# Kernel tuning notes

Measured on AMD Instinct MI355X. Metric: run time of the kernel, lower is better.

The kernel has to match this reference:

```python
import jax, jax.numpy as jnp
import numpy as np

B, N, D, KD = 8, 2048, 64, 64

def setup_inputs() -> dict:
    key = jax.random.key(0)
    ks = jax.random.split(key, 7)
    s = 1.0 / np.sqrt(D)
    return {
        "x":  jax.random.normal(ks[0], (B, N, D), dtype=jnp.float32),
        "Wq": jax.random.normal(ks[1], (D, KD), dtype=jnp.float32) * s,
        "bq": jnp.zeros((KD,), jnp.float32),
        "Wk": jax.random.normal(ks[2], (D, KD), dtype=jnp.float32) * s,
        "bk": jnp.zeros((KD,), jnp.float32),
        "Wv": jax.random.normal(ks[3], (D, KD), dtype=jnp.float32) * s,
        "bv": jnp.zeros((KD,), jnp.float32),
    }

def reference(x, Wq, bq, Wk, bk, Wv, bv):
    # Q,K,V: [B,N,KD]
    Q = x @ Wq + bq
    K = x @ Wk + bk
    V = x @ Wv + bv
    # scores: [B,N,N] (note: original applies NO 1/sqrt(d) scaling)
    scores = jnp.einsum('bij,bkj->bik', Q, K)
    probs = jax.nn.softmax(scores, axis=-1)
    # mean-threshold sparsification: keep entries above the row mean
    mask = (probs > jnp.mean(probs, axis=-1, keepdims=True)).astype(probs.dtype)
    sparse = probs * mask
    out = jnp.einsum('bij,bjk->bik', sparse, V)  # [B,N,KD]
    return out
```

## Files before the change

### kernel.cpp

```cpp
#include <hip/hip_runtime.h>

#define NB 8
#define NS 2048
#define ND 64
#define LOG2E 1.44269504f

typedef _Float16 half8 __attribute__((ext_vector_type(8)));
typedef _Float16 half4 __attribute__((ext_vector_type(4)));
typedef __attribute__((ext_vector_type(4))) float floatx4;

__device__ __forceinline__ half8 cvt8(const float* p) {
    float4 a = *(const float4*)p;
    float4 b = *(const float4*)(p + 4);
    half8 h = {(_Float16)a.x, (_Float16)a.y, (_Float16)a.z, (_Float16)a.w,
               (_Float16)b.x, (_Float16)b.y, (_Float16)b.z, (_Float16)b.w};
    return h;
}

__global__ __launch_bounds__(256) void wprep(
    const float* __restrict__ Wq, const float* __restrict__ Wk,
    const float* __restrict__ Wv, _Float16* __restrict__ Wt)
{
    const int m = blockIdx.x;
    const float* W = (m == 0) ? Wq : (m == 1) ? Wk : Wv;
    for (int i = threadIdx.x; i < 64 * 64; i += 256) {
        const int c = i >> 6, d = i & 63;
        Wt[((size_t)m * 64 + c) * 64 + d] = (_Float16)W[d * 64 + c];
    }
}

__global__ __launch_bounds__(256) void qkv_proj(
    const float* __restrict__ x, const _Float16* __restrict__ Wt,
    const float* __restrict__ bq, const float* __restrict__ bk,
    const float* __restrict__ bv,
    _Float16* __restrict__ Qg, _Float16* __restrict__ Kg,
    _Float16* __restrict__ Vt)
{
    __shared__ _Float16 vt[4][64 * 20];

    const int tid  = threadIdx.x;
    const int wv   = tid >> 6;
    const int l    = tid & 63;
    const int quad = l >> 4;
    const int tx   = l & 15;

    const int b  = blockIdx.x & 7;
    const int n0 = (blockIdx.x >> 3) * 64 + wv * 16;

    const float* xr = x + ((size_t)b * NS + n0 + tx) * ND + quad * 8;
    half8 a0 = cvt8(xr);
    half8 a1 = cvt8(xr + 32);

    const floatx4 zf = {0.f, 0.f, 0.f, 0.f};

#pragma unroll
    for (int ctile = 0; ctile < 12; ++ctile) {
        const int m    = ctile >> 2;
        const int lcol = (ctile & 3) * 16 + tx;

        const _Float16* Wb = Wt + ((size_t)m * 64 + lcol) * 64;
        half8 b0 = *(const half8*)(Wb + quad * 8);
        half8 b1 = *(const half8*)(Wb + 32 + quad * 8);

        floatx4 acc = __builtin_amdgcn_mfma_f32_16x16x32_f16(a0, b0, zf, 0, 0, 0);
        acc = __builtin_amdgcn_mfma_f32_16x16x32_f16(a1, b1, acc, 0, 0, 0);

        const float* Bp = (m == 0) ? bq : (m == 1) ? bk : bv;
        const float bias = Bp[lcol];

        if (m == 0) {
#pragma unroll
            for (int r = 0; r < 4; ++r)
                Qg[((size_t)b * NS + n0 + quad * 4 + r) * ND + lcol] =
                    (_Float16)((acc[r] + bias) * LOG2E);
        } else if (m == 1) {
#pragma unroll
            for (int r = 0; r < 4; ++r)
                Kg[((size_t)b * NS + n0 + quad * 4 + r) * ND + lcol] =
                    (_Float16)(acc[r] + bias);
        } else {
#pragma unroll
            for (int r = 0; r < 4; ++r)
                vt[wv][lcol * 20 + quad * 4 + r] = (_Float16)(acc[r] + bias);
        }
    }
    __syncthreads();
    {
        const int d = l;
        const _Float16* src = &vt[wv][d * 20];
        uint2 p0 = *(const uint2*)(src);
        uint2 p1 = *(const uint2*)(src + 4);
        uint2 p2 = *(const uint2*)(src + 8);
        uint2 p3 = *(const uint2*)(src + 12);
        uint4 q0 = {p0.x, p0.y, p1.x, p1.y};
        uint4 q1 = {p2.x, p2.y, p3.x, p3.y};
        _Float16* dst = Vt + ((size_t)b * ND + d) * NS + n0;
        *(uint4*)(dst)     = q0;
        *(uint4*)(dst + 8) = q1;
    }
}

__global__ __launch_bounds__(512, 2) void attn(
    const _Float16* __restrict__ Qg,
    const _Float16* __restrict__ Kg,
    const _Float16* __restrict__ Vt,
    float* __restrict__ out)
{
    __shared__ __align__(16) _Float16 smem[2 * 64 * 72 + 2 * 64 * 72];
    __shared__ float lsh[4 * 64];

    _Float16* ksm = smem;
    _Float16* vsm = smem + 2 * 64 * 72;

    const int tid  = threadIdx.x;
    const int wv   = tid >> 6;
    const int l    = tid & 63;
    const int quad = l >> 4;
    const int tx   = l & 15;
    const int h    = wv >> 2;
    const int kq   = wv & 3;

    const int b  = blockIdx.x & 7;
    const int q0 = (blockIdx.x >> 3) * 64;

    const _Float16* Qb = Qg + ((size_t)b * NS + q0 + h * 32) * ND;
    const _Float16* Kb = Kg + (size_t)b * NS * ND;
    const _Float16* Vb = Vt + (size_t)b * ND * NS;

    half8 qf[2][2];
#pragma unroll
    for (int rh = 0; rh < 2; ++rh)
#pragma unroll
        for (int kc = 0; kc < 2; ++kc)
            qf[rh][kc] = *(const half8*)(Qb + (size_t)(rh * 16 + tx) * ND + kc * 32 + quad * 8);

    const int skey = tid >> 3;
    const int sc   = (tid & 7) * 8;
    const _Float16* Ksrc = Kb + (size_t)skey * ND + sc;
    const _Float16* Vsrc = Vb + (size_t)skey * NS + sc;
    const int kdst = skey * 72 + sc;

    const floatx4 zf = {0.f, 0.f, 0.f, 0.f};
    const int krow = (kq * 16 + tx) * 72;

    float lacc0 = 0.f, lacc1 = 0.f;
    {
        uint4 gk = *(const uint4*)Ksrc;
        *(uint4*)(ksm + kdst) = gk;
        for (int t = 0; t < 32; ++t) {
            const int buf = (t & 1) * 4608;
            __syncthreads();
            if (t < 31) gk = *(const uint4*)(Ksrc + (size_t)(t + 1) * 64 * ND);
            half8 kf0 = *(const half8*)(ksm + buf + krow + quad * 8);
            half8 kf1 = *(const half8*)(ksm + buf + krow + 32 + quad * 8);
#pragma unroll
            for (int rh = 0; rh < 2; ++rh) {
                floatx4 c = __builtin_amdgcn_mfma_f32_16x16x32_f16(kf0, qf[rh][0], zf, 0, 0, 0);
                c = __builtin_amdgcn_mfma_f32_16x16x32_f16(kf1, qf[rh][1], c, 0, 0, 0);
                float ladd = __builtin_amdgcn_exp2f(c[0]) + __builtin_amdgcn_exp2f(c[1])
                           + __builtin_amdgcn_exp2f(c[2]) + __builtin_amdgcn_exp2f(c[3]);
                if (rh == 0) lacc0 += ladd; else lacc1 += ladd;
            }
            if (t < 31) *(uint4*)(ksm + (buf ^ 4608) + kdst) = gk;
        }
    }
#pragma unroll
    for (int off = 16; off < 64; off <<= 1) {
        lacc0 += __shfl_xor(lacc0, off);
        lacc1 += __shfl_xor(lacc1, off);
    }
    if (quad == 0) {
        lsh[kq * 64 + h * 32 + tx]      = lacc0;
        lsh[kq * 64 + h * 32 + 16 + tx] = lacc1;
    }

    uint4 gk = *(const uint4*)Ksrc;
    uint4 gv = *(const uint4*)Vsrc;
    __syncthreads();

    float thr0, inv0, thr1, inv1;
    {
        const int row = h * 32 + tx;
        float L0 = lsh[row] + lsh[64 + row] + lsh[128 + row] + lsh[192 + row];
        float L1 = lsh[row + 16] + lsh[64 + row + 16] + lsh[128 + row + 16] + lsh[192 + row + 16];
        inv0 = 1.f / L0;  thr0 = L0 * (1.f / (float)NS);
        inv1 = 1.f / L1;  thr1 = L1 * (1.f / (float)NS);
    }

    *(uint4*)(ksm + kdst) = gk;
    *(uint4*)(vsm + kdst) = gv;

    floatx4 o[2][4] = {{zf, zf, zf, zf}, {zf, zf, zf, zf}};

    for (int t = 0; t < 32; ++t) {
        const int buf = (t & 1) * 4608;
        __syncthreads();
        if (t < 31) {
            gk = *(const uint4*)(Ksrc + (size_t)(t + 1) * 64 * ND);
            gv = *(const uint4*)(Vsrc + (size_t)(t + 1) * 64);
        }
        half8 kf0 = *(const half8*)(ksm + buf + krow + quad * 8);
        half8 kf1 = *(const half8*)(ksm + buf + krow + 32 + quad * 8);
        half4 vf[4];
#pragma unroll
        for (int dg = 0; dg < 4; ++dg)
            vf[dg] = *(const half4*)(vsm + buf + (dg * 16 + tx) * 72 + kq * 16 + quad * 4);
#pragma unroll
        for (int rh = 0; rh < 2; ++rh) {
            floatx4 c = __builtin_amdgcn_mfma_f32_16x16x32_f16(kf0, qf[rh][0], zf, 0, 0, 0);
            c = __builtin_amdgcn_mfma_f32_16x16x32_f16(kf1, qf[rh][1], c, 0, 0, 0);
            const float thr = rh ? thr1 : thr0;
            const float inv = rh ? inv1 : inv0;
            float e0 = __builtin_amdgcn_exp2f(c[0]);
            float e1 = __builtin_amdgcn_exp2f(c[1]);
            float e2 = __builtin_amdgcn_exp2f(c[2]);
            float e3 = __builtin_amdgcn_exp2f(c[3]);
            float w0 = (e0 > thr) ? e0 * inv : 0.f;
            float w1 = (e1 > thr) ? e1 * inv : 0.f;
            float w2 = (e2 > thr) ? e2 * inv : 0.f;
            float w3 = (e3 > thr) ? e3 * inv : 0.f;
            half4 af = {(_Float16)w0, (_Float16)w1, (_Float16)w2, (_Float16)w3};
#pragma unroll
            for (int dg = 0; dg < 4; ++dg)
                o[rh][dg] = __builtin_amdgcn_mfma_f32_16x16x16f16(af, vf[dg], o[rh][dg], 0, 0, 0);
        }
        if (t < 31) {
            *(uint4*)(ksm + (buf ^ 4608) + kdst) = gk;
            *(uint4*)(vsm + (buf ^ 4608) + kdst) = gv;
        }
    }

    __syncthreads();
    float* osm = (float*)smem;
    if (kq == 0) {
#pragma unroll
        for (int rh = 0; rh < 2; ++rh)
#pragma unroll
            for (int dg = 0; dg < 4; ++dg)
#pragma unroll
                for (int r = 0; r < 4; ++r)
                    osm[(h * 32 + rh * 16 + quad * 4 + r) * 68 + dg * 16 + tx] = o[rh][dg][r];
    }
    __syncthreads();
    if (kq == 1) {
#pragma unroll
        for (int rh = 0; rh < 2; ++rh)
#pragma unroll
            for (int dg = 0; dg < 4; ++dg)
#pragma unroll
                for (int r = 0; r < 4; ++r)
                    osm[(h * 32 + rh * 16 + quad * 4 + r) * 68 + dg * 16 + tx] += o[rh][dg][r];
    }
    __syncthreads();
    if (kq == 2) {
#pragma unroll
        for (int rh = 0; rh < 2; ++rh)
#pragma unroll
            for (int dg = 0; dg < 4; ++dg)
#pragma unroll
                for (int r = 0; r < 4; ++r)
                    osm[(h * 32 + rh * 16 + quad * 4 + r) * 68 + dg * 16 + tx] += o[rh][dg][r];
    }
    __syncthreads();
    if (kq == 3) {
#pragma unroll
        for (int rh = 0; rh < 2; ++rh)
#pragma unroll
            for (int dg = 0; dg < 4; ++dg)
#pragma unroll
                for (int r = 0; r < 4; ++r)
                    out[((size_t)b * NS + q0 + h * 32 + rh * 16 + quad * 4 + r) * ND + dg * 16 + tx] =
                        osm[(h * 32 + rh * 16 + quad * 4 + r) * 68 + dg * 16 + tx] + o[rh][dg][r];
    }
}

extern "C" void kernel_launch(void* const* d_in, const int* in_sizes, int n_in,
                              void* d_out, int out_size, void* d_ws, size_t ws_size,
                              hipStream_t stream) {
    const float* x  = (const float*)d_in[0];
    const float* Wq = (const float*)d_in[1];
    const float* bq = (const float*)d_in[2];
    const float* Wk = (const float*)d_in[3];
    const float* bk = (const float*)d_in[4];
    const float* Wv = (const float*)d_in[5];
    const float* bv = (const float*)d_in[6];

    _Float16* Qg = (_Float16*)d_ws;
    _Float16* Kg = Qg + (size_t)NB * NS * ND;
    _Float16* Vt = Kg + (size_t)NB * NS * ND;
    _Float16* Wt = Vt + (size_t)NB * NS * ND;

    wprep<<<3, 256, 0, stream>>>(Wq, Wk, Wv, Wt);
    qkv_proj<<<NB * (NS / 64), 256, 0, stream>>>(x, Wt, bq, bk, bv, Qg, Kg, Vt);
    attn<<<NB * (NS / 64), 512, 0, stream>>>(Qg, Kg, Vt, (float*)d_out);
}
```

Measured before the change: 112.4 us.

## Cache quantized scores in LDS to skip recomputing QK^T in second pass

The first pass now stores each wave's attention scores as 16-bit fixed-point integers (scale 256) in a per-wave LDS buffer. The second pass reads them back instead of recomputing Q·K^T. K and V are loaded straight from global memory into registers with double-buffered prefetch rather than staged through shared LDS tiles, and each block handles 32 query rows with 8 waves splitting the keys. This removes the second QK MFMA pass and the per-tile barriers, at the cost of about 135KB of LDS per block (likely one block per CU), quantization error in the scores, a clamp at ±125 in the log2 domain, and a tree reduction across 8 waves.

```diff
diff --git a/kernel.cpp b/kernel.cpp
--- a/kernel.cpp
+++ b/kernel.cpp
@@ -4,6 +4,8 @@
 #define NS 2048
 #define ND 64
 #define LOG2E 1.44269504f
+#define QSC 256.0f
+#define IQS (1.0f / 256.0f)
 
 typedef _Float16 half8 __attribute__((ext_vector_type(8)));
 typedef _Float16 half4 __attribute__((ext_vector_type(4)));
@@ -106,26 +108,24 @@
     const _Float16* __restrict__ Vt,
     float* __restrict__ out)
 {
-    __shared__ __align__(16) _Float16 smem[2 * 64 * 72 + 2 * 64 * 72];
-    __shared__ float lsh[4 * 64];
-
-    _Float16* ksm = smem;
-    _Float16* vsm = smem + 2 * 64 * 72;
+    __shared__ short psl[8][32 * 264];
+    __shared__ float lsh[32 * 8];
 
     const int tid  = threadIdx.x;
     const int wv   = tid >> 6;
     const int l    = tid & 63;
     const int quad = l >> 4;
     const int tx   = l & 15;
-    const int h    = wv >> 2;
+    const int e    = wv >> 2;
     const int kq   = wv & 3;
 
     const int b  = blockIdx.x & 7;
-    const int q0 = (blockIdx.x >> 3) * 64;
-
-    const _Float16* Qb = Qg + ((size_t)b * NS + q0 + h * 32) * ND;
+    const int q0 = (blockIdx.x >> 3) * 32;
+
+    const _Float16* Qb = Qg + ((size_t)b * NS + q0) * ND;
     const _Float16* Kb = Kg + (size_t)b * NS * ND;
     const _Float16* Vb = Vt + (size_t)b * ND * NS;
+    short* ps = psl[wv];
 
     half8 qf[2][2];
 #pragma unroll
@@ -134,34 +134,44 @@
         for (int kc = 0; kc < 2; ++kc)
             qf[rh][kc] = *(const half8*)(Qb + (size_t)(rh * 16 + tx) * ND + kc * 32 + quad * 8);
 
-    const int skey = tid >> 3;
-    const int sc   = (tid & 7) * 8;
-    const _Float16* Ksrc = Kb + (size_t)skey * ND + sc;
-    const _Float16* Vsrc = Vb + (size_t)skey * NS + sc;
-    const int kdst = skey * 72 + sc;
-
     const floatx4 zf = {0.f, 0.f, 0.f, 0.f};
-    const int krow = (kq * 16 + tx) * 72;
+
+    const _Float16* Kw = Kb + ((size_t)(e * 64 + kq * 16 + tx)) * ND;
 
     float lacc0 = 0.f, lacc1 = 0.f;
     {
-        uint4 gk = *(const uint4*)Ksrc;
-        *(uint4*)(ksm + kdst) = gk;
-        for (int t = 0; t < 32; ++t) {
-            const int buf = (t & 1) * 4608;
-            __syncthreads();
-            if (t < 31) gk = *(const uint4*)(Ksrc + (size_t)(t + 1) * 64 * ND);
-            half8 kf0 = *(const half8*)(ksm + buf + krow + quad * 8);
-            half8 kf1 = *(const half8*)(ksm + buf + krow + 32 + quad * 8);
+        half8 kf0[2], kf1[2];
+        kf0[0] = *(const half8*)(Kw + quad * 8);
+        kf1[0] = *(const half8*)(Kw + 32 + quad * 8);
+        kf0[1] = *(const half8*)(Kw + (size_t)128 * ND + quad * 8);
+        kf1[1] = *(const half8*)(Kw + (size_t)128 * ND + 32 + quad * 8);
+#pragma unroll
+        for (int tl = 0; tl < 16; ++tl) {
+            const int sl = tl & 1;
+            half8 a0 = kf0[sl], a1 = kf1[sl];
+            if (tl < 14) {
+                kf0[sl] = *(const half8*)(Kw + (size_t)(tl + 2) * 128 * ND + quad * 8);
+                kf1[sl] = *(const half8*)(Kw + (size_t)(tl + 2) * 128 * ND + 32 + quad * 8);
+            }
 #pragma unroll
             for (int rh = 0; rh < 2; ++rh) {
-                floatx4 c = __builtin_amdgcn_mfma_f32_16x16x32_f16(kf0, qf[rh][0], zf, 0, 0, 0);
-                c = __builtin_amdgcn_mfma_f32_16x16x32_f16(kf1, qf[rh][1], c, 0, 0, 0);
-                float ladd = __builtin_amdgcn_exp2f(c[0]) + __builtin_amdgcn_exp2f(c[1])
-                           + __builtin_amdgcn_exp2f(c[2]) + __builtin_amdgcn_exp2f(c[3]);
+                floatx4 c = __builtin_amdgcn_mfma_f32_16x16x32_f16(a0, qf[rh][0], zf, 0, 0, 0);
+                c = __builtin_amdgcn_mfma_f32_16x16x32_f16(a1, qf[rh][1], c, 0, 0, 0);
+                int ic[4];
+                float ladd = 0.f;
+#pragma unroll
+                for (int r = 0; r < 4; ++r) {
+                    float cs = fminf(fmaxf(c[r] * QSC, -32000.f), 32000.f);
+                    int v = (int)rintf(cs);
+                    ic[r] = v;
+                    ladd += __builtin_amdgcn_exp2f((float)v * IQS);
+                }
                 if (rh == 0) lacc0 += ladd; else lacc1 += ladd;
-            }
-            if (t < 31) *(uint4*)(ksm + (buf ^ 4608) + kdst) = gk;
+                uint2 pk;
+                pk.x = (unsigned)(ic[0] & 0xffff) | ((unsigned)ic[1] << 16);
+                pk.y = (unsigned)(ic[2] & 0xffff) | ((unsigned)ic[3] << 16);
+                *(uint2*)&ps[(rh * 16 + tx) * 264 + tl * 16 + quad * 4] = pk;
+            }
         }
     }
 #pragma unroll
@@ -170,107 +180,152 @@
         lacc1 += __shfl_xor(lacc1, off);
     }
     if (quad == 0) {
-        lsh[kq * 64 + h * 32 + tx]      = lacc0;
-        lsh[kq * 64 + h * 32 + 16 + tx] = lacc1;
-    }
-
-    uint4 gk = *(const uint4*)Ksrc;
-    uint4 gv = *(const uint4*)Vsrc;
+        lsh[tx * 8 + wv]        = lacc0;
+        lsh[(16 + tx) * 8 + wv] = lacc1;
+    }
     __syncthreads();
 
     float thr0, inv0, thr1, inv1;
     {
-        const int row = h * 32 + tx;
-        float L0 = lsh[row] + lsh[64 + row] + lsh[128 + row] + lsh[192 + row];
-        float L1 = lsh[row + 16] + lsh[64 + row + 16] + lsh[128 + row + 16] + lsh[192 + row + 16];
+        float4 s0a = *(const float4*)&lsh[tx * 8];
+        float4 s0b = *(const float4*)&lsh[tx * 8 + 4];
+        float4 s1a = *(const float4*)&lsh[(16 + tx) * 8];
+        float4 s1b = *(const float4*)&lsh[(16 + tx) * 8 + 4];
+        float L0 = s0a.x + s0a.y + s0a.z + s0a.w + s0b.x + s0b.y + s0b.z + s0b.w;
+        float L1 = s1a.x + s1a.y + s1a.z + s1a.w + s1b.x + s1b.y + s1b.z + s1b.w;
         inv0 = 1.f / L0;  thr0 = L0 * (1.f / (float)NS);
         inv1 = 1.f / L1;  thr1 = L1 * (1.f / (float)NS);
     }
 
-    *(uint4*)(ksm + kdst) = gk;
-    *(uint4*)(vsm + kdst) = gv;
+    const _Float16* Vw = Vb + (size_t)tx * NS + e * 64 + kq * 16 + quad * 4;
 
     floatx4 o[2][4] = {{zf, zf, zf, zf}, {zf, zf, zf, zf}};
-
-    for (int t = 0; t < 32; ++t) {
-        const int buf = (t & 1) * 4608;
-        __syncthreads();
-        if (t < 31) {
-            gk = *(const uint4*)(Ksrc + (size_t)(t + 1) * 64 * ND);
-            gv = *(const uint4*)(Vsrc + (size_t)(t + 1) * 64);
+    {
+        uint2 P0[2], P1[2];
+        half4 Vf[2][4];
+        P0[0] = *(const uint2*)&ps[tx * 264 + quad * 4];
+        P1[0] = *(const uint2*)&ps[(16 + tx) * 264 + quad * 4];
+        P0[1] = *(const uint2*)&ps[tx * 264 + 16 + quad * 4];
+        P1[1] = *(const uint2*)&ps[(16 + tx) * 264 + 16 + quad * 4];
+#pragma unroll
+        for (int dg = 0; dg < 4; ++dg) {
+            Vf[0][dg] = *(const half4*)(Vw + (size_t)(dg * 16) * NS);
+            Vf[1][dg] = *(const half4*)(Vw + (size_t)(dg * 16) * NS + 128);
         }
-        half8 kf0 = *(const half8*)(ksm + buf + krow + quad * 8);
-        half8 kf1 = *(const half8*)(ksm + buf + krow + 32 + quad * 8);
-        half4 vf[4];
-#pragma unroll
-        for (int dg = 0; dg < 4; ++dg)
-            vf[dg] = *(const half4*)(vsm + buf + (dg * 16 + tx) * 72 + kq * 16 + quad * 4);
-#pragma unroll
-        for (int rh = 0; rh < 2; ++rh) {
-            floatx4 c = __builtin_amdgcn_mfma_f32_16x16x32_f16(kf0, qf[rh][0], zf, 0, 0, 0);
-            c = __builtin_amdgcn_mfma_f32_16x16x32_f16(kf1, qf[rh][1], c, 0, 0, 0);
-            const float thr = rh ? thr1 : thr0;
-            const float inv = rh ? inv1 : inv0;
-            float e0 = __builtin_amdgcn_exp2f(c[0]);
-            float e1 = __builtin_amdgcn_exp2f(c[1]);
-            float e2 = __builtin_amdgcn_exp2f(c[2]);
-            float e3 = __builtin_amdgcn_exp2f(c[3]);
-            float w0 = (e0 > thr) ? e0 * inv : 0.f;
-            float w1 = (e1 > thr) ? e1 * inv : 0.f;
-            float w2 = (e2 > thr) ? e2 * inv : 0.f;
-            float w3 = (e3 > thr) ? e3 * inv : 0.f;
-            half4 af = {(_Float16)w0, (_Float16)w1, (_Float16)w2, (_Float16)w3};
-#pragma unroll
-            for (int dg = 0; dg < 4; ++dg)
-                o[rh][dg] = __builtin_amdgcn_mfma_f32_16x16x16f16(af, vf[dg], o[rh][dg], 0, 0, 0);
+#pragma unroll
+        for (int tl = 0; tl < 16; ++tl) {
+            const int sl = tl & 1;
+            uint2 u0 = P0[sl], u1 = P1[sl];
+            half4 v0 = Vf[sl][0], v1 = Vf[sl][1], v2 = Vf[sl][2], v3 = Vf[sl][3];
+            if (tl < 14) {
+                P0[sl] = *(const uint2*)&ps[tx * 264 + (tl + 2) * 16 + quad * 4];
+                P1[sl] = *(const uint2*)&ps[(16 + tx) * 264 + (tl + 2) * 16 + quad * 4];
+#pragma unroll
+                for (int dg = 0; dg < 4; ++dg)
+                    Vf[sl][dg] = *(const half4*)(Vw + (size_t)(dg * 16) * NS + (tl + 2) * 128);
+            }
+            half4 af0, af1;
+            {
+                int s0 = (int)(short)(u0.x), s1 = (int)(short)(u0.x >> 16);
+                int s2 = (int)(short)(u0.y), s3 = (int)(short)(u0.y >> 16);
+                float e0 = __builtin_amdgcn_exp2f((float)s0 * IQS);
+                float e1 = __builtin_amdgcn_exp2f((float)s1 * IQS);
+                float e2 = __builtin_amdgcn_exp2f((float)s2 * IQS);
+                float e3 = __builtin_amdgcn_exp2f((float)s3 * IQS);
+                af0[0] = (_Float16)((e0 > thr0) ? e0 * inv0 : 0.f);
+                af0[1] = (_Float16)((e1 > thr0) ? e1 * inv0 : 0.f);
+                af0[2] = (_Float16)((e2 > thr0) ? e2 * inv0 : 0.f);
+                af0[3] = (_Float16)((e3 > thr0) ? e3 * inv0 : 0.f);
+            }
+            {
+                int s0 = (int)(short)(u1.x), s1 = (int)(short)(u1.x >> 16);
+                int s2 = (int)(short)(u1.y), s3 = (int)(short)(u1.y >> 16);
+                float e0 = __builtin_amdgcn_exp2f((float)s0 * IQS);
+                float e1 = __builtin_amdgcn_exp2f((float)s1 * IQS);
+                float e2 = __builtin_amdgcn_exp2f((float)s2 * IQS);
+                float e3 = __builtin_amdgcn_exp2f((float)s3 * IQS);
+                af1[0] = (_Float16)((e0 > thr1) ? e0 * inv1 : 0.f);
+                af1[1] = (_Float16)((e1 > thr1) ? e1 * inv1 : 0.f);
+                af1[2] = (_Float16)((e2 > thr1) ? e2 * inv1 : 0.f);
+                af1[3] = (_Float16)((e3 > thr1) ? e3 * inv1 : 0.f);
+            }
+            o[0][0] = __builtin_amdgcn_mfma_f32_16x16x16f16(af0, v0, o[0][0], 0, 0, 0);
+            o[0][1] = __builtin_amdgcn_mfma_f32_16x16x16f16(af0, v1, o[0][1], 0, 0, 0);
+            o[0][2] = __builtin_amdgcn_mfma_f32_16x16x16f16(af0, v2, o[0][2], 0, 0, 0);
+            o[0][3] = __builtin_amdgcn_mfma_f32_16x16x16f16(af0, v3, o[0][3], 0, 0, 0);
+            o[1][0] = __builtin_amdgcn_mfma_f32_16x16x16f16(af1, v0, o[1][0], 0, 0, 0);
+            o[1][1] = __builtin_amdgcn_mfma_f32_16x16x16f16(af1, v1, o[1][1], 0, 0, 0);
+            o[1][2] = __builtin_amdgcn_mfma_f32_16x16x16f16(af1, v2, o[1][2], 0, 0, 0);
+            o[1][3] = __builtin_amdgcn_mfma_f32_16x16x16f16(af1, v3, o[1][3], 0, 0, 0);
         }
-        if (t < 31) {
-            *(uint4*)(ksm + (buf ^ 4608) + kdst) = gk;
-            *(uint4*)(vsm + (buf ^ 4608) + kdst) = gv;
-        }
-    }
-
-    __syncthreads();
-    float* osm = (float*)smem;
-    if (kq == 0) {
-#pragma unroll
-        for (int rh = 0; rh < 2; ++rh)
-#pragma unroll
-            for (int dg = 0; dg < 4; ++dg)
-#pragma unroll
-                for (int r = 0; r < 4; ++r)
-                    osm[(h * 32 + rh * 16 + quad * 4 + r) * 68 + dg * 16 + tx] = o[rh][dg][r];
-    }
-    __syncthreads();
-    if (kq == 1) {
-#pragma unroll
-        for (int rh = 0; rh < 2; ++rh)
-#pragma unroll
-            for (int dg = 0; dg < 4; ++dg)
-#pragma unroll
-                for (int r = 0; r < 4; ++r)
-                    osm[(h * 32 + rh * 16 + quad * 4 + r) * 68 + dg * 16 + tx] += o[rh][dg][r];
-    }
-    __syncthreads();
-    if (kq == 2) {
-#pragma unroll
-        for (int rh = 0; rh < 2; ++rh)
-#pragma unroll
-            for (int dg = 0; dg < 4; ++dg)
-#pragma unroll
-                for (int r = 0; r < 4; ++r)
-                    osm[(h * 32 + rh * 16 + quad * 4 + r) * 68 + dg * 16 + tx] += o[rh][dg][r];
-    }
-    __syncthreads();
-    if (kq == 3) {
-#pragma unroll
-        for (int rh = 0; rh < 2; ++rh)
-#pragma unroll
-            for (int dg = 0; dg < 4; ++dg)
-#pragma unroll
-                for (int r = 0; r < 4; ++r)
-                    out[((size_t)b * NS + q0 + h * 32 + rh * 16 + quad * 4 + r) * ND + dg * 16 + tx] =
-                        osm[(h * 32 + rh * 16 + quad * 4 + r) * 68 + dg * 16 + tx] + o[rh][dg][r];
+    }
+
+    __syncthreads();
+    float* osm = (float*)&psl[0][0];
+    if (wv >= 4) {
+        float* s = osm + (size_t)(wv - 4) * 32 * 68;
+#pragma unroll
+        for (int rh = 0; rh < 2; ++rh)
+#pragma unroll
+            for (int dg = 0; dg < 4; ++dg)
+#pragma unroll
+                for (int r = 0; r < 4; ++r)
+                    s[(rh * 16 + quad * 4 + r) * 68 + dg * 16 + tx] = o[rh][dg][r];
+    }
+    __syncthreads();
+    if (wv < 4) {
+        const float* s = osm + (size_t)wv * 32 * 68;
+#pragma unroll
+        for (int rh = 0; rh < 2; ++rh)
+#pragma unroll
+            for (int dg = 0; dg < 4; ++dg)
+#pragma unroll
+                for (int r = 0; r < 4; ++r)
+                    o[rh][dg][r] += s[(rh * 16 + quad * 4 + r) * 68 + dg * 16 + tx];
+    }
+    __syncthreads();
+    if (wv == 2 || wv == 3) {
+        float* s = osm + (size_t)(wv - 2) * 32 * 68;
+#pragma unroll
+        for (int rh = 0; rh < 2; ++rh)
+#pragma unroll
+            for (int dg = 0; dg < 4; ++dg)
+#pragma unroll
+                for (int r = 0; r < 4; ++r)
+                    s[(rh * 16 + quad * 4 + r) * 68 + dg * 16 + tx] = o[rh][dg][r];
+    }
+    __syncthreads();
+    if (wv < 2) {
+        const float* s = osm + (size_t)wv * 32 * 68;
+#pragma unroll
+        for (int rh = 0; rh < 2; ++rh)
+#pragma unroll
+            for (int dg = 0; dg < 4; ++dg)
+#pragma unroll
+                for (int r = 0; r < 4; ++r)
+                    o[rh][dg][r] += s[(rh * 16 + quad * 4 + r) * 68 + dg * 16 + tx];
+    }
+    __syncthreads();
+    if (wv == 1) {
+        float* s = osm;
+#pragma unroll
+        for (int rh = 0; rh < 2; ++rh)
+#pragma unroll
+            for (int dg = 0; dg < 4; ++dg)
+#pragma unroll
+                for (int r = 0; r < 4; ++r)
+                    s[(rh * 16 + quad * 4 + r) * 68 + dg * 16 + tx] = o[rh][dg][r];
+    }
+    __syncthreads();
+    if (wv == 0) {
+#pragma unroll
+        for (int rh = 0; rh < 2; ++rh)
+#pragma unroll
+            for (int dg = 0; dg < 4; ++dg)
+#pragma unroll
+                for (int r = 0; r < 4; ++r)
+                    out[((size_t)b * NS + q0 + rh * 16 + quad * 4 + r) * ND + dg * 16 + tx] =
+                        o[rh][dg][r] + osm[(rh * 16 + quad * 4 + r) * 68 + dg * 16 + tx];
     }
 }
 
@@ -292,5 +347,5 @@
 
     wprep<<<3, 256, 0, stream>>>(Wq, Wk, Wv, Wt);
     qkv_proj<<<NB * (NS / 64), 256, 0, stream>>>(x, Wt, bq, bk, bv, Qg, Kg, Vt);
-    attn<<<NB * (NS / 64), 512, 0, stream>>>(Qg, Kg, Vt, (float*)d_out);
-}
+    attn<<<NB * (NS / 32), 512, 0, stream>>>(Qg, Kg, Vt, (float*)d_out);
+}
```

Result: slower. 127.4 us (+13.4%).

## Halve query tile per block and XOR-swizzle K/V shared memory

Applied to the files above, without the earlier changes.

The attention kernel now handles 32 query rows per block instead of 64, which doubles the grid to 512 blocks and has each wave own a single 16-row slice. That should spread work across more CUs, but each K/V tile is now loaded from global memory by twice as many blocks. K and V tiles are stored in shared memory with an XOR swizzle on 8-element chunks, with matching swizzled read offsets, to reduce LDS bank conflicts. Per-thread registers drop because the accumulators and Q fragments shrink by half.

```diff
diff --git a/kernel.cpp b/kernel.cpp
--- a/kernel.cpp
+++ b/kernel.cpp
@@ -107,7 +107,7 @@
     float* __restrict__ out)
 {
     __shared__ __align__(16) _Float16 smem[2 * 64 * 72 + 2 * 64 * 72];
-    __shared__ float lsh[4 * 64];
+    __shared__ float lsh[4 * 32];
 
     _Float16* ksm = smem;
     _Float16* vsm = smem + 2 * 64 * 72;
@@ -117,80 +117,74 @@
     const int l    = tid & 63;
     const int quad = l >> 4;
     const int tx   = l & 15;
-    const int h    = wv >> 2;
+    const int rh   = wv >> 2;
     const int kq   = wv & 3;
 
     const int b  = blockIdx.x & 7;
-    const int q0 = (blockIdx.x >> 3) * 64;
-
-    const _Float16* Qb = Qg + ((size_t)b * NS + q0 + h * 32) * ND;
+    const int q0 = (blockIdx.x >> 3) * 32;
+
+    const _Float16* Qb = Qg + ((size_t)b * NS + q0 + rh * 16) * ND;
     const _Float16* Kb = Kg + (size_t)b * NS * ND;
     const _Float16* Vb = Vt + (size_t)b * ND * NS;
 
-    half8 qf[2][2];
-#pragma unroll
-    for (int rh = 0; rh < 2; ++rh)
-#pragma unroll
-        for (int kc = 0; kc < 2; ++kc)
-            qf[rh][kc] = *(const half8*)(Qb + (size_t)(rh * 16 + tx) * ND + kc * 32 + quad * 8);
+    half8 qf[2];
+#pragma unroll
+    for (int kc = 0; kc < 2; ++kc)
+        qf[kc] = *(const half8*)(Qb + (size_t)tx * ND + kc * 32 + quad * 8);
 
     const int skey = tid >> 3;
-    const int sc   = (tid & 7) * 8;
-    const _Float16* Ksrc = Kb + (size_t)skey * ND + sc;
-    const _Float16* Vsrc = Vb + (size_t)skey * NS + sc;
-    const int kdst = skey * 72 + sc;
+    const int sc   = tid & 7;
+    const _Float16* Ksrc = Kb + (size_t)skey * ND + sc * 8;
+    const _Float16* Vsrc = Vb + (size_t)skey * NS + sc * 8;
+    const int sdst = skey * 72 + ((sc ^ (skey & 7)) * 8);
 
     const floatx4 zf = {0.f, 0.f, 0.f, 0.f};
-    const int krow = (kq * 16 + tx) * 72;
-
-    float lacc0 = 0.f, lacc1 = 0.f;
+    const int t7    = tx & 7;
+    const int krow  = (kq * 16 + tx) * 72;
+    const int koff0 = (quad ^ t7) * 8;
+    const int koff1 = ((quad ^ 4) ^ t7) * 8;
+
+    float lacc = 0.f;
     {
         uint4 gk = *(const uint4*)Ksrc;
-        *(uint4*)(ksm + kdst) = gk;
+        *(uint4*)(ksm + sdst) = gk;
         for (int t = 0; t < 32; ++t) {
             const int buf = (t & 1) * 4608;
             __syncthreads();
             if (t < 31) gk = *(const uint4*)(Ksrc + (size_t)(t + 1) * 64 * ND);
-            half8 kf0 = *(const half8*)(ksm + buf + krow + quad * 8);
-            half8 kf1 = *(const half8*)(ksm + buf + krow + 32 + quad * 8);
-#pragma unroll
-            for (int rh = 0; rh < 2; ++rh) {
-                floatx4 c = __builtin_amdgcn_mfma_f32_16x16x32_f16(kf0, qf[rh][0], zf, 0, 0, 0);
-                c = __builtin_amdgcn_mfma_f32_16x16x32_f16(kf1, qf[rh][1], c, 0, 0, 0);
-                float ladd = __builtin_amdgcn_exp2f(c[0]) + __builtin_amdgcn_exp2f(c[1])
-                           + __builtin_amdgcn_exp2f(c[2]) + __builtin_amdgcn_exp2f(c[3]);
-                if (rh == 0) lacc0 += ladd; else lacc1 += ladd;
-            }
-            if (t < 31) *(uint4*)(ksm + (buf ^ 4608) + kdst) = gk;
-        }
-    }
-#pragma unroll
-    for (int off = 16; off < 64; off <<= 1) {
-        lacc0 += __shfl_xor(lacc0, off);
-        lacc1 += __shfl_xor(lacc1, off);
-    }
-    if (quad == 0) {
-        lsh[kq * 64 + h * 32 + tx]      = lacc0;
-        lsh[kq * 64 + h * 32 + 16 + tx] = lacc1;
-    }
+            half8 kf0 = *(const half8*)(ksm + buf + krow + koff0);
+            half8 kf1 = *(const half8*)(ksm + buf + krow + koff1);
+            floatx4 c = __builtin_amdgcn_mfma_f32_16x16x32_f16(kf0, qf[0], zf, 0, 0, 0);
+            c = __builtin_amdgcn_mfma_f32_16x16x32_f16(kf1, qf[1], c, 0, 0, 0);
+            lacc += __builtin_amdgcn_exp2f(c[0]) + __builtin_amdgcn_exp2f(c[1])
+                  + __builtin_amdgcn_exp2f(c[2]) + __builtin_amdgcn_exp2f(c[3]);
+            if (t < 31) *(uint4*)(ksm + (buf ^ 4608) + sdst) = gk;
+        }
+    }
+#pragma unroll
+    for (int off = 16; off < 64; off <<= 1)
+        lacc += __shfl_xor(lacc, off);
+    if (quad == 0)
+        lsh[kq * 32 + rh * 16 + tx] = lacc;
 
     uint4 gk = *(const uint4*)Ksrc;
     uint4 gv = *(const uint4*)Vsrc;
     __syncthreads();
 
-    float thr0, inv0, thr1, inv1;
+    float thr, inv;
     {
-        const int row = h * 32 + tx;
-        float L0 = lsh[row] + lsh[64 + row] + lsh[128 + row] + lsh[192 + row];
-        float L1 = lsh[row + 16] + lsh[64 + row + 16] + lsh[128 + row + 16] + lsh[192 + row + 16];
-        inv0 = 1.f / L0;  thr0 = L0 * (1.f / (float)NS);
-        inv1 = 1.f / L1;  thr1 = L1 * (1.f / (float)NS);
-    }
-
-    *(uint4*)(ksm + kdst) = gk;
-    *(uint4*)(vsm + kdst) = gv;
-
-    floatx4 o[2][4] = {{zf, zf, zf, zf}, {zf, zf, zf, zf}};
+        const int row = rh * 16 + tx;
+        float L = lsh[row] + lsh[32 + row] + lsh[64 + row] + lsh[96 + row];
+        inv = 1.f / L;
+        thr = L * (1.f / (float)NS);
+    }
+
+    *(uint4*)(ksm + sdst) = gk;
+    *(uint4*)(vsm + sdst) = gv;
+
+    const int vchunk = ((kq * 2 + (quad >> 1)) ^ t7) * 8 + (quad & 1) * 4;
+
+    floatx4 o[4] = {zf, zf, zf, zf};
 
     for (int t = 0; t < 32; ++t) {
         const int buf = (t & 1) * 4608;
@@ -199,78 +193,68 @@
             gk = *(const uint4*)(Ksrc + (size_t)(t + 1) * 64 * ND);
             gv = *(const uint4*)(Vsrc + (size_t)(t + 1) * 64);
         }
-        half8 kf0 = *(const half8*)(ksm + buf + krow + quad * 8);
-        half8 kf1 = *(const half8*)(ksm + buf + krow + 32 + quad * 8);
+        half8 kf0 = *(const half8*)(ksm + buf + krow + koff0);
+        half8 kf1 = *(const half8*)(ksm + buf + krow + koff1);
         half4 vf[4];
 #pragma unroll
         for (int dg = 0; dg < 4; ++dg)
-            vf[dg] = *(const half4*)(vsm + buf + (dg * 16 + tx) * 72 + kq * 16 + quad * 4);
-#pragma unroll
-        for (int rh = 0; rh < 2; ++rh) {
-            floatx4 c = __builtin_amdgcn_mfma_f32_16x16x32_f16(kf0, qf[rh][0], zf, 0, 0, 0);
-            c = __builtin_amdgcn_mfma_f32_16x16x32_f16(kf1, qf[rh][1], c, 0, 0, 0);
-            const float thr = rh ? thr1 : thr0;
-            const float inv = rh ? inv1 : inv0;
-            float e0 = __builtin_amdgcn_exp2f(c[0]);
-            float e1 = __builtin_amdgcn_exp2f(c[1]);
-            float e2 = __builtin_amdgcn_exp2f(c[2]);
-            float e3 = __builtin_amdgcn_exp2f(c[3]);
-            float w0 = (e0 > thr) ? e0 * inv : 0.f;
-            float w1 = (e1 > thr) ? e1 * inv : 0.f;
-            float w2 = (e2 > thr) ? e2 * inv : 0.f;
-            float w3 = (e3 > thr) ? e3 * inv : 0.f;
-            half4 af = {(_Float16)w0, (_Float16)w1, (_Float16)w2, (_Float16)w3};
-#pragma unroll
-            for (int dg = 0; dg < 4; ++dg)
-                o[rh][dg] = __builtin_amdgcn_mfma_f32_16x16x16f16(af, vf[dg], o[rh][dg], 0, 0, 0);
-        }
+            vf[dg] = *(const half4*)(vsm + buf + (dg * 16 + tx) * 72 + vchunk);
+
+        floatx4 c = __builtin_amdgcn_mfma_f32_16x16x32_f16(kf0, qf[0], zf, 0, 0, 0);
+        c = __builtin_amdgcn_mfma_f32_16x16x32_f16(kf1, qf[1], c, 0, 0, 0);
+        float e0 = __builtin_amdgcn_exp2f(c[0]);
+        float e1 = __builtin_amdgcn_exp2f(c[1]);
+        float e2 = __builtin_amdgcn_exp2f(c[2]);
+        float e3 = __builtin_amdgcn_exp2f(c[3]);
+        float w0 = (e0 > thr) ? e0 * inv : 0.f;
+        float w1 = (e1 > thr) ? e1 * inv : 0.f;
+        float w2 = (e2 > thr) ? e2 * inv : 0.f;
+        float w3 = (e3 > thr) ? e3 * inv : 0.f;
+        half4 af = {(_Float16)w0, (_Float16)w1, (_Float16)w2, (_Float16)w3};
+#pragma unroll
+        for (int dg = 0; dg < 4; ++dg)
+            o[dg] = __builtin_amdgcn_mfma_f32_16x16x16f16(af, vf[dg], o[dg], 0, 0, 0);
+
         if (t < 31) {
-            *(uint4*)(ksm + (buf ^ 4608) + kdst) = gk;
-            *(uint4*)(vsm + (buf ^ 4608) + kdst) = gv;
+            *(uint4*)(ksm + (buf ^ 4608) + sdst) = gk;
+            *(uint4*)(vsm + (buf ^ 4608) + sdst) = gv;
         }
     }
 
     __syncthreads();
     float* osm = (float*)smem;
+    const int orow = rh * 16 + quad * 4;
     if (kq == 0) {
 #pragma unroll
-        for (int rh = 0; rh < 2; ++rh)
-#pragma unroll
-            for (int dg = 0; dg < 4; ++dg)
-#pragma unroll
-                for (int r = 0; r < 4; ++r)
-                    osm[(h * 32 + rh * 16 + quad * 4 + r) * 68 + dg * 16 + tx] = o[rh][dg][r];
+        for (int dg = 0; dg < 4; ++dg)
+#pragma unroll
+            for (int r = 0; r < 4; ++r)
+                osm[(orow + r) * 68 + dg * 16 + tx] = o[dg][r];
     }
     __syncthreads();
     if (kq == 1) {
 #pragma unroll
-        for (int rh = 0; rh < 2; ++rh)
-#pragma unroll
-            for (int dg = 0; dg < 4; ++dg)
-#pragma unroll
-                for (int r = 0; r < 4; ++r)
-                    osm[(h * 32 + rh * 16 + quad * 4 + r) * 68 + dg * 16 + tx] += o[rh][dg][r];
+        for (int dg = 0; dg < 4; ++dg)
+#pragma unroll
+            for (int r = 0; r < 4; ++r)
+                osm[(orow + r) * 68 + dg * 16 + tx] += o[dg][r];
     }
     __syncthreads();
     if (kq == 2) {
 #pragma unroll
-        for (int rh = 0; rh < 2; ++rh)
-#pragma unroll
-            for (int dg = 0; dg < 4; ++dg)
-#pragma unroll
-                for (int r = 0; r < 4; ++r)
-                    osm[(h * 32 + rh * 16 + quad * 4 + r) * 68 + dg * 16 + tx] += o[rh][dg][r];
+        for (int dg = 0; dg < 4; ++dg)
+#pragma unroll
+            for (int r = 0; r < 4; ++r)
+                osm[(orow + r) * 68 + dg * 16 + tx] += o[dg][r];
     }
     __syncthreads();
     if (kq == 3) {
 #pragma unroll
-        for (int rh = 0; rh < 2; ++rh)
-#pragma unroll
-            for (int dg = 0; dg < 4; ++dg)
-#pragma unroll
-                for (int r = 0; r < 4; ++r)
-                    out[((size_t)b * NS + q0 + h * 32 + rh * 16 + quad * 4 + r) * ND + dg * 16 + tx] =
-                        osm[(h * 32 + rh * 16 + quad * 4 + r) * 68 + dg * 16 + tx] + o[rh][dg][r];
+        for (int dg = 0; dg < 4; ++dg)
+#pragma unroll
+            for (int r = 0; r < 4; ++r)
+                out[((size_t)b * NS + q0 + orow + r) * ND + dg * 16 + tx] =
+                    osm[(orow + r) * 68 + dg * 16 + tx] + o[dg][r];
     }
 }
 
@@ -292,5 +276,5 @@
 
     wprep<<<3, 256, 0, stream>>>(Wq, Wk, Wv, Wt);
     qkv_proj<<<NB * (NS / 64), 256, 0, stream>>>(x, Wt, bq, bk, bv, Qg, Kg, Vt);
-    attn<<<NB * (NS / 64), 512, 0, stream>>>(Qg, Kg, Vt, (float*)d_out);
-}
+    attn<<<NB * (NS / 32), 512, 0, stream>>>(Qg, Kg, Vt, (float*)d_out);
+}
```

Result: no change. 113.5 us (+1.0%).
